# Kernel tuning notes

Measured on AMD Instinct MI355X. Metric: run time of the kernel, lower is better.

The kernel has to match this reference:

```python
import jax, jax.numpy as jnp
import numpy as np

EMBED_DIM = 1024
NUM_HEADS = 16
HEAD_DIM = EMBED_DIM // NUM_HEADS
BATCH = 2
SEQ = 2048


def setup_inputs() -> dict:
    key = jax.random.key(0)
    ks = jax.random.split(key, 10)
    s = 1.0 / np.sqrt(EMBED_DIM)
    inp = {
        "query": jax.random.normal(ks[0], (BATCH, SEQ, EMBED_DIM), jnp.float32),
        # Linear weights stored as [in, out] (y = x @ W + b)
        "wq": jax.random.normal(ks[1], (EMBED_DIM, EMBED_DIM), jnp.float32) * s,
        "bq": jnp.zeros((EMBED_DIM,), jnp.float32),
        "wk": jax.random.normal(ks[2], (EMBED_DIM, EMBED_DIM), jnp.float32) * s,
        "bk": jnp.zeros((EMBED_DIM,), jnp.float32),
        "wv": jax.random.normal(ks[3], (EMBED_DIM, EMBED_DIM), jnp.float32) * s,
        "bv": jnp.zeros((EMBED_DIM,), jnp.float32),
        "wo": jax.random.normal(ks[4], (EMBED_DIM, EMBED_DIM), jnp.float32) * s,
        "bo": jnp.zeros((EMBED_DIM,), jnp.float32),
        "temperature": jnp.float32(HEAD_DIM),  # learnable temperature, init = head_dim
    }
    return inp


def reference(query, wq, bq, wk, bk, wv, bv, wo, bo, temperature):
    B, S, E = query.shape
    # self-attention: key = value = query
    Q = (query @ wq + bq).reshape(B, S, NUM_HEADS, HEAD_DIM).transpose(0, 2, 1, 3)
    K = (query @ wk + bk).reshape(B, S, NUM_HEADS, HEAD_DIM).transpose(0, 2, 1, 3)
    V = (query @ wv + bv).reshape(B, S, NUM_HEADS, HEAD_DIM).transpose(0, 2, 1, 3)
    # squared Euclidean distances: ||q||^2 + ||k||^2 - 2<q,k>
    q_sq = jnp.sum(Q * Q, axis=-1, keepdims=True)          # (B,H,Sq,1)
    k_sq = jnp.sum(K * K, axis=-1, keepdims=True)          # (B,H,Sk,1)
    qk = jnp.einsum("bhqd,bhkd->bhqk", Q, K)
    d_sq = jnp.maximum(q_sq + jnp.swapaxes(k_sq, -2, -1) - 2.0 * qk, 0.0)
    attn = jax.nn.softmax(-d_sq / temperature, axis=-1)    # (B,H,Sq,Sk)
    out = jnp.einsum("bhqk,bhkd->bhqd", attn, V)
    out = out.transpose(0, 2, 1, 3).reshape(B, S, E)
    return out @ wo + bo
```

## Files before the change

### kernel.cpp

```cpp
#include <hip/hip_runtime.h>
#include <stdint.h>
#include <stddef.h>


#define LOG2E 1.44269504088896f

typedef __attribute__((ext_vector_type(8))) short bf16x8;
typedef __attribute__((ext_vector_type(4))) float f32x4;
typedef __attribute__((ext_vector_type(4))) unsigned short u16x4;

__device__ __forceinline__ unsigned short f2b(float f) {
  union { float f; unsigned int u; } x; x.f = f;
  unsigned int u = x.u;
  u += 0x7fffu + ((u >> 16) & 1u);
  return (unsigned short)(u >> 16);
}
__device__ __forceinline__ float b2f(unsigned short s) {
  union { unsigned int u; float f; } x; x.u = ((unsigned int)s) << 16;
  return x.f;
}
__device__ __forceinline__ unsigned int fbits(float f) {
  union { float f; unsigned int u; } x; x.f = f; return x.u;
}

#define GLD_LDS(g, l) __builtin_amdgcn_global_load_lds( \
    (const __attribute__((address_space(1))) void*)(g), \
    (__attribute__((address_space(3))) void*)(l), 16, 0, 0)

__global__ void prep_kernel(const float* __restrict__ X,
                            const float* __restrict__ wq, const float* __restrict__ wk,
                            const float* __restrict__ wv, const float* __restrict__ wo,
                            unsigned short* __restrict__ Xb,
                            unsigned short* __restrict__ WTqkv, unsigned short* __restrict__ WTo) {
  int z = blockIdx.z;
  if (z == 4) {
    size_t base = ((size_t)(blockIdx.y * 16 + blockIdx.x)) * 16384;
    #pragma unroll
    for (int j = 0; j < 16; ++j) {
      size_t i = base + (size_t)(j * 256 + threadIdx.x) * 4;
      f32x4 v = *(const f32x4*)&X[i];
      u16x4 o;
      #pragma unroll
      for (int k = 0; k < 4; ++k) o[k] = f2b(v[k]);
      *(u16x4*)&Xb[i] = o;
    }
    return;
  }
  __shared__ float tile[64][65];
  const float* src = (z == 0) ? wq : (z == 1) ? wk : (z == 2) ? wv : wo;
  unsigned short* dst = (z < 3) ? (WTqkv + (size_t)z * 1024 * 1024) : WTo;
  int k0 = blockIdx.y * 64, n0 = blockIdx.x * 64;
  int rr = threadIdx.x >> 6, cc = threadIdx.x & 63;
  #pragma unroll
  for (int p = 0; p < 16; ++p) {
    int row = p * 4 + rr;
    tile[row][cc] = src[(size_t)(k0 + row) * 1024 + n0 + cc];
  }
  __syncthreads();
  #pragma unroll
  for (int p = 0; p < 16; ++p) {
    int row = p * 4 + rr;
    dst[(size_t)(n0 + row) * 1024 + k0 + cc] = f2b(tile[cc][row]);
  }
}

__global__ __launch_bounds__(256, 3) void gemm_qkv_kernel(
    const unsigned short* __restrict__ X, const unsigned short* __restrict__ WT,
    const float* __restrict__ bq, const float* __restrict__ bk, const float* __restrict__ bv,
    const float* __restrict__ temp,
    unsigned short* __restrict__ Qb, unsigned short* __restrict__ Kb,
    unsigned short* __restrict__ VTo, float* __restrict__ ks2) {
  __shared__ __align__(16) unsigned short smem[16896];
  unsigned short* As = smem;
  unsigned short* Bs = smem + 8192;
  const int t = threadIdx.x, w = t >> 6, lane = t & 63;
  const int r = lane & 15, q4 = lane >> 4;
  const int m0 = blockIdx.y * 128, n0 = blockIdx.x * 128;
  const int wr = (w >> 1) * 64, wc = (w & 1) * 64;
  const unsigned short* Xg = X + (size_t)m0 * 1024;
  const unsigned short* Wg = WT + (size_t)n0 * 1024;
  f32x4 acc[4][4] = {};
  for (int k0 = 0; k0 < 1024; k0 += 64) {
    #pragma unroll
    for (int g = 0; g < 4; ++g) {
      int slot = g * 256 + t;
      int kh = slot >> 9, row = (slot >> 2) & 127, ko = (slot & 3) * 8;
      GLD_LDS(Xg + (size_t)row * 1024 + k0 + kh * 32 + ko, &As[(g * 256 + w * 64) * 8]);
      GLD_LDS(Wg + (size_t)row * 1024 + k0 + kh * 32 + ko, &Bs[(g * 256 + w * 64) * 8]);
    }
    __syncthreads();
    #pragma unroll
    for (int kh = 0; kh < 2; ++kh) {
      bf16x8 af[4], bfr[4];
      #pragma unroll
      for (int mf = 0; mf < 4; ++mf)
        af[mf] = *(const bf16x8*)&As[kh * 4096 + (wr + mf * 16 + r) * 32 + q4 * 8];
      #pragma unroll
      for (int nf = 0; nf < 4; ++nf)
        bfr[nf] = *(const bf16x8*)&Bs[kh * 4096 + (wc + nf * 16 + r) * 32 + q4 * 8];
      #pragma unroll
      for (int mf = 0; mf < 4; ++mf)
        #pragma unroll
        for (int nf = 0; nf < 4; ++nf)
          acc[mf][nf] = __builtin_amdgcn_mfma_f32_16x16x32_bf16(af[mf], bfr[nf], acc[mf][nf], 0, 0, 0);
    }
    __syncthreads();
  }
  const int nblk = n0 >> 10;
  if (nblk == 0) {
    const int nc0 = n0 & 1023;
    #pragma unroll
    for (int nf = 0; nf < 4; ++nf) {
      int n = nc0 + wc + nf * 16 + r;
      float bb = bq[n];
      #pragma unroll
      for (int mf = 0; mf < 4; ++mf) {
        int m = m0 + wr + mf * 16 + q4 * 4;
        f32x4 v = acc[mf][nf];
        #pragma unroll
        for (int i = 0; i < 4; ++i)
          Qb[(size_t)(m + i) * 1024 + n] = f2b(v[i] + bb);
      }
    }
  } else if (nblk == 1) {
    const float sc = LOG2E / temp[0];
    const int nc0 = n0 & 1023;
    float s2a[4][4] = {};
    #pragma unroll
    for (int nf = 0; nf < 4; ++nf) {
      int n = nc0 + wc + nf * 16 + r;
      float bb = bk[n];
      #pragma unroll
      for (int mf = 0; mf < 4; ++mf) {
        int m = m0 + wr + mf * 16 + q4 * 4;
        f32x4 v = acc[mf][nf];
        #pragma unroll
        for (int i = 0; i < 4; ++i) {
          unsigned short os = f2b(v[i] + bb);
          Kb[(size_t)(m + i) * 1024 + n] = os;
          float xb = b2f(os);
          s2a[mf][i] += xb * xb;
        }
      }
    }
    #pragma unroll
    for (int mf = 0; mf < 4; ++mf)
      #pragma unroll
      for (int i = 0; i < 4; ++i) {
        float v = s2a[mf][i];
        v += __shfl_xor(v, 1, 64);
        v += __shfl_xor(v, 2, 64);
        v += __shfl_xor(v, 4, 64);
        v += __shfl_xor(v, 8, 64);
        s2a[mf][i] = v * sc;
      }
    if (r == 0) {
      int hh = (nc0 + wc) >> 6;
      #pragma unroll
      for (int mf = 0; mf < 4; ++mf) {
        int m = m0 + wr + mf * 16 + q4 * 4;
        int bb2 = m >> 11, ss = m & 2047;
        #pragma unroll
        for (int i = 0; i < 4; ++i)
          ks2[(size_t)(bb2 * 16 + hh) * 2048 + ss + i] = s2a[mf][i];
      }
    }
  } else {
    unsigned short* Vt = smem;
    const int c0 = n0 - 2048;
    const int head = w & 1;
    #pragma unroll
    for (int nf = 0; nf < 4; ++nf) {
      int c = c0 + wc + nf * 16 + r;
      float bb = bv[c];
      int d = c & 63;
      #pragma unroll
      for (int mf = 0; mf < 4; ++mf) {
        int mloc = wr + mf * 16 + q4 * 4;
        int G = mloc >> 6;
        int k6 = mloc & 63;
        int pos = (k6 >> 5) * 32 + ((k6 & 15) >> 2) * 8 + ((k6 >> 4) & 1) * 4;
        f32x4 v = acc[mf][nf];
        u16x4 pk;
        #pragma unroll
        for (int i = 0; i < 4; ++i) pk[i] = f2b(v[i] + bb);
        *(u16x4*)&Vt[(head * 64 + d) * 132 + G * 64 + pos] = pk;
      }
    }
    __syncthreads();
    int row = t >> 1, ch = t & 1;
    int hd = row >> 6, dd = row & 63;
    int hglob = (c0 >> 6) + hd;
    int bb2 = m0 >> 11, s0 = m0 & 2047;
    unsigned short* dst = &VTo[((size_t)((bb2 * 16 + hglob) * 64 + dd)) * 2048 + s0 + ch * 64];
    const unsigned short* srcL = &Vt[(hd * 64 + dd) * 132 + ch * 64];
    #pragma unroll
    for (int k2 = 0; k2 < 16; ++k2)
      *(u16x4*)&dst[k2 * 4] = *(const u16x4*)&srcL[k2 * 4];
  }
}

__global__ __launch_bounds__(256, 2) void flash_kernel(
    const unsigned short* __restrict__ Qb, const unsigned short* __restrict__ Kb,
    const unsigned short* __restrict__ VT, const float* __restrict__ ks2,
    const float* __restrict__ temp, unsigned short* __restrict__ AO) {
  __shared__ __align__(16) unsigned short Ks[2][64 * 64];
  __shared__ __align__(16) unsigned short Vs[3][64 * 64];
  __shared__ __align__(16) float KQs[2048];
  const int t = threadIdx.x, w = t >> 6, lane = t & 63;
  const int r = lane & 15, q4 = lane >> 4;
  const int wgid = blockIdx.x + 16 * blockIdx.y;
  const int xcd = wgid & 7, s = wgid >> 3;
  const int bh = xcd + 8 * (s & 3);
  const int b = bh >> 4, h = bh & 15;
  const int q0 = (s >> 2) * 128;
  const float cc = 2.0f * LOG2E / temp[0];

  bf16x8 qf[2][2];
  #pragma unroll
  for (int qg = 0; qg < 2; ++qg) {
    int sq = q0 + w * 32 + qg * 16 + r;
    const unsigned short* qp = Qb + (size_t)(b * 2048 + sq) * 1024 + h * 64;
    #pragma unroll
    for (int ks = 0; ks < 2; ++ks) qf[qg][ks] = *(const bf16x8*)(qp + ks * 32 + q4 * 8);
  }

  f32x4 accO[2][4] = {};
  f32x4 lsum[2] = {};
  bf16x8 ones;
  #pragma unroll
  for (int j = 0; j < 8; ++j) ones[j] = (short)0x3F80;

  const unsigned short* Kg = Kb + ((size_t)b * 2048) * 1024 + h * 64;
  const unsigned short* Vg = VT + ((size_t)bh * 64) * 2048;
  const float* kqb = ks2 + bh * 2048;

  const unsigned short* kp0 = Kg + (size_t)(t >> 2) * 1024 + (t & 3) * 8;
  const unsigned short* kp1 = kp0 + 32;
  int dd0 = t >> 3;
  const unsigned short* vp0 = Vg + (size_t)dd0 * 2048 + ((t & 7) ^ (dd0 & 7)) * 8;
  const unsigned short* vp1 = vp0 + (size_t)32 * 2048;

  GLD_LDS(kqb + t * 4, &KQs[t * 4]);
  GLD_LDS(kqb + 1024 + t * 4, &KQs[1024 + t * 4]);
  GLD_LDS(kp0, &Ks[0][t * 8]);
  GLD_LDS(kp1, &Ks[0][(256 + t) * 8]);
  GLD_LDS(vp0, &Vs[0][t * 8]);
  GLD_LDS(vp1, &Vs[0][(256 + t) * 8]);
  kp0 += 65536; kp1 += 65536; vp0 += 64; vp1 += 64;
  GLD_LDS(kp0, &Ks[1][t * 8]);
  GLD_LDS(kp1, &Ks[1][(256 + t) * 8]);
  GLD_LDS(vp0, &Vs[1][t * 8]);
  GLD_LDS(vp1, &Vs[1][(256 + t) * 8]);
  kp0 += 65536; kp1 += 65536; vp0 += 64; vp1 += 64;

  const unsigned short* v_cur = &Vs[0][0];
  const unsigned short* v_nxt = &Vs[1][0];
  const unsigned short* v_fre = &Vs[2][0];

  asm volatile("s_waitcnt vmcnt(4)" ::: "memory");
  __builtin_amdgcn_s_barrier();
  __builtin_amdgcn_sched_barrier(0);

  f32x4 stA[2][4], stB[2][4];
  {
    const f32x4 zz = {};
    __builtin_amdgcn_s_setprio(1);
    #pragma unroll
    for (int ks = 0; ks < 2; ++ks) {
      #pragma unroll
      for (int kfm = 0; kfm < 4; ++kfm) {
        bf16x8 ka = *(const bf16x8*)&Ks[0][(ks * 64 + kfm * 16 + r) * 32 + q4 * 8];
        stA[0][kfm] = __builtin_amdgcn_mfma_f32_16x16x32_bf16(ka, qf[0][ks], ks ? stA[0][kfm] : zz, 0, 0, 0);
        stA[1][kfm] = __builtin_amdgcn_mfma_f32_16x16x32_bf16(ka, qf[1][ks], ks ? stA[1][kfm] : zz, 0, 0, 0);
      }
    }
    __builtin_amdgcn_s_setprio(0);
  }

#define CHUNK_BODY(C, STC, STN)                                               \
  {                                                                           \
    const int c_ = (C);                                                       \
    __builtin_amdgcn_s_barrier();                                             \
    if (c_ < 30) {                                                            \
      unsigned short* kdst = &Ks[(C) & 1][0];                                 \
      GLD_LDS(kp0, kdst + t * 8);                                             \
      GLD_LDS(kp1, kdst + (256 + t) * 8);                                     \
      GLD_LDS(vp0, (unsigned short*)v_fre + t * 8);                           \
      GLD_LDS(vp1, (unsigned short*)v_fre + (256 + t) * 8);                   \
      kp0 += 65536; kp1 += 65536; vp0 += 64; vp1 += 64;                       \
      asm volatile("s_waitcnt vmcnt(4)" ::: "memory");                        \
    } else {                                                                  \
      asm volatile("s_waitcnt vmcnt(0)" ::: "memory");                        \
    }                                                                         \
    __builtin_amdgcn_s_barrier();                                             \
    __builtin_amdgcn_sched_barrier(0);                                        \
                 \
    if (c_ < 31) {                                                            \
      const unsigned short* krd = &Ks[((C) + 1) & 1][0];                      \
      const f32x4 zz = {};                                                    \
      __builtin_amdgcn_s_setprio(1);                                          \
      _Pragma("unroll")                                                       \
      for (int ks = 0; ks < 2; ++ks) {                                        \
        _Pragma("unroll")                                                     \
        for (int kfm = 0; kfm < 4; ++kfm) {                                   \
          bf16x8 ka = *(const bf16x8*)&krd[(ks * 64 + kfm * 16 + r) * 32 + q4 * 8]; \
          STN[0][kfm] = __builtin_amdgcn_mfma_f32_16x16x32_bf16(ka, qf[0][ks], ks ? STN[0][kfm] : zz, 0, 0, 0); \
          STN[1][kfm] = __builtin_amdgcn_mfma_f32_16x16x32_bf16(ka, qf[1][ks], ks ? STN[1][kfm] : zz, 0, 0, 0); \
        }                                                                     \
      }                                                                       \
      __builtin_amdgcn_s_setprio(0);                                          \
    }                                                                         \
                                \
    f32x4 kq[4];                                                              \
    _Pragma("unroll")                                                         \
    for (int kfm = 0; kfm < 4; ++kfm)                                         \
      kq[kfm] = *(const f32x4*)&KQs[c_ * 64 + kfm * 16 + q4 * 4];             \
    bf16x8 pf[2][2];                                                          \
    _Pragma("unroll")                                                         \
    for (int qg = 0; qg < 2; ++qg) {                                          \
      _Pragma("unroll")                                                       \
      for (int cb = 0; cb < 2; ++cb) {                                        \
        unsigned int dw[4];                                                   \
        _Pragma("unroll")                                                     \
        for (int half = 0; half < 2; ++half) {                                \
          int kfm = cb * 2 + half;                                            \
          float pp[4];                                                        \
          _Pragma("unroll")                                                   \
          for (int i = 0; i < 4; ++i) {                                       \
            float u = __builtin_fmaf(cc, STC[qg][kfm][i], -kq[kfm][i]);       \
            pp[i] = __builtin_amdgcn_exp2f(u);                                \
          }                                                                   \
          dw[half * 2 + 0] = (fbits(pp[0]) >> 16) | (fbits(pp[1]) & 0xFFFF0000u); \
          dw[half * 2 + 1] = (fbits(pp[2]) >> 16) | (fbits(pp[3]) & 0xFFFF0000u); \
        }                                                                     \
        union { unsigned int d[4]; bf16x8 v; } cv;                            \
        cv.d[0] = dw[0]; cv.d[1] = dw[1]; cv.d[2] = dw[2]; cv.d[3] = dw[3];   \
        pf[qg][cb] = cv.v;                                                    \
      }                                                                       \
    }                                                                         \
        \
    __builtin_amdgcn_s_setprio(1);                                            \
    _Pragma("unroll")                                                         \
    for (int cb = 0; cb < 2; ++cb) {                                          \
      lsum[0] = __builtin_amdgcn_mfma_f32_16x16x32_bf16(pf[0][cb], ones, lsum[0], 0, 0, 0); \
      lsum[1] = __builtin_amdgcn_mfma_f32_16x16x32_bf16(pf[1][cb], ones, lsum[1], 0, 0, 0); \
      _Pragma("unroll")                                                       \
      for (int df = 0; df < 4; ++df) {                                        \
        int dloc = df * 16 + r;                                               \
        int un = dloc * 8 + ((cb * 4 + q4) ^ (dloc & 7));                     \
        bf16x8 vb = *(const bf16x8*)&v_cur[un * 8];                           \
        accO[0][df] = __builtin_amdgcn_mfma_f32_16x16x32_bf16(pf[0][cb], vb, accO[0][df], 0, 0, 0); \
        accO[1][df] = __builtin_amdgcn_mfma_f32_16x16x32_bf16(pf[1][cb], vb, accO[1][df], 0, 0, 0); \
      }                                                                       \
    }                                                                         \
    __builtin_amdgcn_s_setprio(0);                                            \
                                                        \
    const unsigned short* tv = v_cur; v_cur = v_nxt; v_nxt = v_fre; v_fre = tv; \
  }

  for (int c2 = 0; c2 < 16; ++c2) {
    CHUNK_BODY(2 * c2, stA, stB)
    CHUNK_BODY(2 * c2 + 1, stB, stA)
  }
#undef CHUNK_BODY

  {
    #pragma unroll
    for (int qg = 0; qg < 2; ++qg) {
      float inv[4];
      #pragma unroll
      for (int i = 0; i < 4; ++i) inv[i] = 1.0f / lsum[qg][i];
      #pragma unroll
      for (int df = 0; df < 4; ++df) {
        int d = df * 16 + r;
        #pragma unroll
        for (int i = 0; i < 4; ++i) {
          int sq = q0 + w * 32 + qg * 16 + q4 * 4 + i;
          AO[(size_t)(b * 2048 + sq) * 1024 + h * 64 + d] = f2b(accO[qg][df][i] * inv[i]);
        }
      }
    }
  }
}

__global__ __launch_bounds__(256, 2) void gemm_out_kernel(
    const unsigned short* __restrict__ A, const unsigned short* __restrict__ WT,
    const float* __restrict__ bo, float* __restrict__ Out) {
  __shared__ __align__(16) unsigned short As[2 * 128 * 32];
  __shared__ __align__(16) unsigned short Bs[2 * 64 * 32];
  const int t = threadIdx.x, w = t >> 6, lane = t & 63;
  const int r = lane & 15, q4 = lane >> 4;
  const int m0 = blockIdx.y * 128, n0 = blockIdx.x * 64;
  const int wr = (w >> 1) * 64, wc = (w & 1) * 32;
  const unsigned short* Ag = A + (size_t)m0 * 1024;
  const unsigned short* Wg = WT + (size_t)n0 * 1024;
  f32x4 acc[4][2] = {};
  for (int k0 = 0; k0 < 1024; k0 += 64) {
    #pragma unroll
    for (int g = 0; g < 4; ++g) {
      int slot = g * 256 + t;
      int kh = slot >> 9, row = (slot >> 2) & 127, ko = (slot & 3) * 8;
      GLD_LDS(Ag + (size_t)row * 1024 + k0 + kh * 32 + ko, &As[(g * 256 + w * 64) * 8]);
    }
    #pragma unroll
    for (int g = 0; g < 2; ++g) {
      int slot = g * 256 + t;
      int kh = slot >> 8, row = (slot >> 2) & 63, ko = (slot & 3) * 8;
      GLD_LDS(Wg + (size_t)row * 1024 + k0 + kh * 32 + ko, &Bs[(g * 256 + w * 64) * 8]);
    }
    __syncthreads();
    #pragma unroll
    for (int kh = 0; kh < 2; ++kh) {
      bf16x8 af[4], bfr[2];
      #pragma unroll
      for (int mf = 0; mf < 4; ++mf)
        af[mf] = *(const bf16x8*)&As[kh * 4096 + (wr + mf * 16 + r) * 32 + q4 * 8];
      #pragma unroll
      for (int nf = 0; nf < 2; ++nf)
        bfr[nf] = *(const bf16x8*)&Bs[kh * 2048 + (wc + nf * 16 + r) * 32 + q4 * 8];
      #pragma unroll
      for (int mf = 0; mf < 4; ++mf)
        #pragma unroll
        for (int nf = 0; nf < 2; ++nf)
          acc[mf][nf] = __builtin_amdgcn_mfma_f32_16x16x32_bf16(af[mf], bfr[nf], acc[mf][nf], 0, 0, 0);
    }
    __syncthreads();
  }
  #pragma unroll
  for (int nf = 0; nf < 2; ++nf) {
    int n = n0 + wc + nf * 16 + r;
    float bb = bo[n];
    #pragma unroll
    for (int mf = 0; mf < 4; ++mf) {
      int m = m0 + wr + mf * 16 + q4 * 4;
      f32x4 v = acc[mf][nf];
      #pragma unroll
      for (int i = 0; i < 4; ++i)
        Out[(size_t)(m + i) * 1024 + n] = v[i] + bb;
    }
  }
}

extern "C" void kernel_launch(void* const* d_in, const int* in_sizes, int n_in,
                              void* d_out, int out_size, void* d_ws, size_t ws_size,
                              hipStream_t stream) {
  const float* X    = (const float*)d_in[0];
  const float* wq   = (const float*)d_in[1];
  const float* bq   = (const float*)d_in[2];
  const float* wk   = (const float*)d_in[3];
  const float* bk   = (const float*)d_in[4];
  const float* wv   = (const float*)d_in[5];
  const float* bv   = (const float*)d_in[6];
  const float* wo   = (const float*)d_in[7];
  const float* bo   = (const float*)d_in[8];
  const float* temp = (const float*)d_in[9];
  float* Out = (float*)d_out;

  char* ws = (char*)d_ws;
  unsigned short* Xb    = (unsigned short*)ws; ws += (size_t)4096 * 1024 * 2;
  unsigned short* WTqkv = (unsigned short*)ws; ws += (size_t)3072 * 1024 * 2;
  unsigned short* WTo   = (unsigned short*)ws; ws += (size_t)1024 * 1024 * 2;
  unsigned short* Qb    = (unsigned short*)ws; ws += (size_t)4096 * 1024 * 2;
  unsigned short* Kb    = (unsigned short*)ws; ws += (size_t)4096 * 1024 * 2;
  unsigned short* VT    = (unsigned short*)ws; ws += (size_t)4096 * 1024 * 2;
  float* ks2 = (float*)ws; ws += (size_t)65536 * 4;
  unsigned short* AO = Xb;

  prep_kernel<<<dim3(16, 16, 5), 256, 0, stream>>>(X, wq, wk, wv, wo, Xb, WTqkv, WTo);
  gemm_qkv_kernel<<<dim3(24, 32), 256, 0, stream>>>(Xb, WTqkv, bq, bk, bv, temp, Qb, Kb, VT, ks2);
  flash_kernel<<<dim3(16, 32), 256, 0, stream>>>(Qb, Kb, VT, ks2, temp, AO);
  gemm_out_kernel<<<dim3(16, 32), 256, 0, stream>>>(AO, WTo, bo, Out);
}
```

Before: 189.1 us.

## Double flash query tile to 256 rows with 4-stage K/V pipeline

The flash kernel now gives each block 256 query rows (64 per wave) instead of 128, which halves the grid and halves how often K/V tiles are reloaded per query. K and V staging moves to a 4-deep ring buffer with 3 chunks prefetched, and the software-pipelined QK^T (computing the next chunk's scores early) is dropped in favour of computing scores within the same chunk. Launch bounds drop to one block per SIMD set, so register pressure and occupancy change. The grid shrinks to 256 blocks, which may underfill the GPU's compute units.

```diff
diff --git a/kernel.cpp b/kernel.cpp
--- a/kernel.cpp
+++ b/kernel.cpp
@@ -200,33 +200,33 @@
   }
 }
 
-__global__ __launch_bounds__(256, 2) void flash_kernel(
+__global__ __launch_bounds__(256, 1) void flash_kernel(
     const unsigned short* __restrict__ Qb, const unsigned short* __restrict__ Kb,
     const unsigned short* __restrict__ VT, const float* __restrict__ ks2,
     const float* __restrict__ temp, unsigned short* __restrict__ AO) {
-  __shared__ __align__(16) unsigned short Ks[2][64 * 64];
-  __shared__ __align__(16) unsigned short Vs[3][64 * 64];
+  __shared__ __align__(16) unsigned short Ks[4][64 * 64];
+  __shared__ __align__(16) unsigned short Vs[4][64 * 64];
   __shared__ __align__(16) float KQs[2048];
   const int t = threadIdx.x, w = t >> 6, lane = t & 63;
   const int r = lane & 15, q4 = lane >> 4;
-  const int wgid = blockIdx.x + 16 * blockIdx.y;
+  const int wgid = blockIdx.x + 8 * blockIdx.y;
   const int xcd = wgid & 7, s = wgid >> 3;
   const int bh = xcd + 8 * (s & 3);
   const int b = bh >> 4, h = bh & 15;
-  const int q0 = (s >> 2) * 128;
+  const int q0 = (s >> 2) * 256;
   const float cc = 2.0f * LOG2E / temp[0];
 
-  bf16x8 qf[2][2];
-  #pragma unroll
-  for (int qg = 0; qg < 2; ++qg) {
-    int sq = q0 + w * 32 + qg * 16 + r;
+  bf16x8 qf[4][2];
+  #pragma unroll
+  for (int qg = 0; qg < 4; ++qg) {
+    int sq = q0 + w * 64 + qg * 16 + r;
     const unsigned short* qp = Qb + (size_t)(b * 2048 + sq) * 1024 + h * 64;
     #pragma unroll
     for (int ks = 0; ks < 2; ++ks) qf[qg][ks] = *(const bf16x8*)(qp + ks * 32 + q4 * 8);
   }
 
-  f32x4 accO[2][4] = {};
-  f32x4 lsum[2] = {};
+  f32x4 accO[4][4] = {};
+  f32x4 lsum[4] = {};
   bf16x8 ones;
   #pragma unroll
   for (int j = 0; j < 8; ++j) ones[j] = (short)0x3F80;
@@ -243,82 +243,51 @@
 
   GLD_LDS(kqb + t * 4, &KQs[t * 4]);
   GLD_LDS(kqb + 1024 + t * 4, &KQs[1024 + t * 4]);
-  GLD_LDS(kp0, &Ks[0][t * 8]);
-  GLD_LDS(kp1, &Ks[0][(256 + t) * 8]);
-  GLD_LDS(vp0, &Vs[0][t * 8]);
-  GLD_LDS(vp1, &Vs[0][(256 + t) * 8]);
-  kp0 += 65536; kp1 += 65536; vp0 += 64; vp1 += 64;
-  GLD_LDS(kp0, &Ks[1][t * 8]);
-  GLD_LDS(kp1, &Ks[1][(256 + t) * 8]);
-  GLD_LDS(vp0, &Vs[1][t * 8]);
-  GLD_LDS(vp1, &Vs[1][(256 + t) * 8]);
-  kp0 += 65536; kp1 += 65536; vp0 += 64; vp1 += 64;
-
-  const unsigned short* v_cur = &Vs[0][0];
-  const unsigned short* v_nxt = &Vs[1][0];
-  const unsigned short* v_fre = &Vs[2][0];
-
-  asm volatile("s_waitcnt vmcnt(4)" ::: "memory");
+  #pragma unroll
+  for (int pc = 0; pc < 3; ++pc) {
+    GLD_LDS(kp0, &Ks[pc][t * 8]);
+    GLD_LDS(kp1, &Ks[pc][(256 + t) * 8]);
+    GLD_LDS(vp0, &Vs[pc][t * 8]);
+    GLD_LDS(vp1, &Vs[pc][(256 + t) * 8]);
+    kp0 += 65536; kp1 += 65536; vp0 += 64; vp1 += 64;
+  }
+  asm volatile("s_waitcnt vmcnt(8)" ::: "memory");
   __builtin_amdgcn_s_barrier();
   __builtin_amdgcn_sched_barrier(0);
 
-  f32x4 stA[2][4], stB[2][4];
-  {
-    const f32x4 zz = {};
-    __builtin_amdgcn_s_setprio(1);
-    #pragma unroll
-    for (int ks = 0; ks < 2; ++ks) {
-      #pragma unroll
-      for (int kfm = 0; kfm < 4; ++kfm) {
-        bf16x8 ka = *(const bf16x8*)&Ks[0][(ks * 64 + kfm * 16 + r) * 32 + q4 * 8];
-        stA[0][kfm] = __builtin_amdgcn_mfma_f32_16x16x32_bf16(ka, qf[0][ks], ks ? stA[0][kfm] : zz, 0, 0, 0);
-        stA[1][kfm] = __builtin_amdgcn_mfma_f32_16x16x32_bf16(ka, qf[1][ks], ks ? stA[1][kfm] : zz, 0, 0, 0);
-      }
-    }
-    __builtin_amdgcn_s_setprio(0);
-  }
-
-#define CHUNK_BODY(C, STC, STN)                                               \
+#define CHUNK_BODY(C, J)                                                      \
   {                                                                           \
     const int c_ = (C);                                                       \
-    __builtin_amdgcn_s_barrier();                                             \
-    if (c_ < 30) {                                                            \
-      unsigned short* kdst = &Ks[(C) & 1][0];                                 \
-      GLD_LDS(kp0, kdst + t * 8);                                             \
-      GLD_LDS(kp1, kdst + (256 + t) * 8);                                     \
-      GLD_LDS(vp0, (unsigned short*)v_fre + t * 8);                           \
-      GLD_LDS(vp1, (unsigned short*)v_fre + (256 + t) * 8);                   \
+    if (c_ < 29) {                                                            \
+      GLD_LDS(kp0, &Ks[((J) + 3) & 3][t * 8]);                                \
+      GLD_LDS(kp1, &Ks[((J) + 3) & 3][(256 + t) * 8]);                        \
+      GLD_LDS(vp0, &Vs[((J) + 3) & 3][t * 8]);                                \
+      GLD_LDS(vp1, &Vs[((J) + 3) & 3][(256 + t) * 8]);                        \
       kp0 += 65536; kp1 += 65536; vp0 += 64; vp1 += 64;                       \
-      asm volatile("s_waitcnt vmcnt(4)" ::: "memory");                        \
-    } else {                                                                  \
-      asm volatile("s_waitcnt vmcnt(0)" ::: "memory");                        \
     }                                                                         \
-    __builtin_amdgcn_s_barrier();                                             \
-    __builtin_amdgcn_sched_barrier(0);                                        \
-                 \
-    if (c_ < 31) {                                                            \
-      const unsigned short* krd = &Ks[((C) + 1) & 1][0];                      \
+         \
+    f32x4 st[4][4];                                                           \
+    {                                                                         \
       const f32x4 zz = {};                                                    \
-      __builtin_amdgcn_s_setprio(1);                                          \
       _Pragma("unroll")                                                       \
       for (int ks = 0; ks < 2; ++ks) {                                        \
         _Pragma("unroll")                                                     \
         for (int kfm = 0; kfm < 4; ++kfm) {                                   \
-          bf16x8 ka = *(const bf16x8*)&krd[(ks * 64 + kfm * 16 + r) * 32 + q4 * 8]; \
-          STN[0][kfm] = __builtin_amdgcn_mfma_f32_16x16x32_bf16(ka, qf[0][ks], ks ? STN[0][kfm] : zz, 0, 0, 0); \
-          STN[1][kfm] = __builtin_amdgcn_mfma_f32_16x16x32_bf16(ka, qf[1][ks], ks ? STN[1][kfm] : zz, 0, 0, 0); \
+          bf16x8 ka = *(const bf16x8*)&Ks[(J)][(ks * 64 + kfm * 16 + r) * 32 + q4 * 8]; \
+          _Pragma("unroll")                                                   \
+          for (int qg = 0; qg < 4; ++qg)                                      \
+            st[qg][kfm] = __builtin_amdgcn_mfma_f32_16x16x32_bf16(ka, qf[qg][ks], ks ? st[qg][kfm] : zz, 0, 0, 0); \
         }                                                                     \
       }                                                                       \
-      __builtin_amdgcn_s_setprio(0);                                          \
     }                                                                         \
-                                \
+                 \
     f32x4 kq[4];                                                              \
     _Pragma("unroll")                                                         \
     for (int kfm = 0; kfm < 4; ++kfm)                                         \
       kq[kfm] = *(const f32x4*)&KQs[c_ * 64 + kfm * 16 + q4 * 4];             \
-    bf16x8 pf[2][2];                                                          \
+    bf16x8 pf[4][2];                                                          \
     _Pragma("unroll")                                                         \
-    for (int qg = 0; qg < 2; ++qg) {                                          \
+    for (int qg = 0; qg < 4; ++qg) {                                          \
       _Pragma("unroll")                                                       \
       for (int cb = 0; cb < 2; ++cb) {                                        \
         unsigned int dw[4];                                                   \
@@ -328,7 +297,7 @@
           float pp[4];                                                        \
           _Pragma("unroll")                                                   \
           for (int i = 0; i < 4; ++i) {                                       \
-            float u = __builtin_fmaf(cc, STC[qg][kfm][i], -kq[kfm][i]);       \
+            float u = __builtin_fmaf(cc, st[qg][kfm][i], -kq[kfm][i]);        \
             pp[i] = __builtin_amdgcn_exp2f(u);                                \
           }                                                                   \
           dw[half * 2 + 0] = (fbits(pp[0]) >> 16) | (fbits(pp[1]) & 0xFFFF0000u); \
@@ -339,35 +308,41 @@
         pf[qg][cb] = cv.v;                                                    \
       }                                                                       \
     }                                                                         \
-        \
-    __builtin_amdgcn_s_setprio(1);                                            \
+         \
     _Pragma("unroll")                                                         \
     for (int cb = 0; cb < 2; ++cb) {                                          \
-      lsum[0] = __builtin_amdgcn_mfma_f32_16x16x32_bf16(pf[0][cb], ones, lsum[0], 0, 0, 0); \
-      lsum[1] = __builtin_amdgcn_mfma_f32_16x16x32_bf16(pf[1][cb], ones, lsum[1], 0, 0, 0); \
+      _Pragma("unroll")                                                       \
+      for (int qg = 0; qg < 4; ++qg)                                          \
+        lsum[qg] = __builtin_amdgcn_mfma_f32_16x16x32_bf16(pf[qg][cb], ones, lsum[qg], 0, 0, 0); \
       _Pragma("unroll")                                                       \
       for (int df = 0; df < 4; ++df) {                                        \
         int dloc = df * 16 + r;                                               \
         int un = dloc * 8 + ((cb * 4 + q4) ^ (dloc & 7));                     \
-        bf16x8 vb = *(const bf16x8*)&v_cur[un * 8];                           \
-        accO[0][df] = __builtin_amdgcn_mfma_f32_16x16x32_bf16(pf[0][cb], vb, accO[0][df], 0, 0, 0); \
-        accO[1][df] = __builtin_amdgcn_mfma_f32_16x16x32_bf16(pf[1][cb], vb, accO[1][df], 0, 0, 0); \
+        bf16x8 vb = *(const bf16x8*)&Vs[(J)][un * 8];                         \
+        _Pragma("unroll")                                                     \
+        for (int qg = 0; qg < 4; ++qg)                                        \
+          accO[qg][df] = __builtin_amdgcn_mfma_f32_16x16x32_bf16(pf[qg][cb], vb, accO[qg][df], 0, 0, 0); \
       }                                                                       \
     }                                                                         \
-    __builtin_amdgcn_s_setprio(0);                                            \
-                                                        \
-    const unsigned short* tv = v_cur; v_cur = v_nxt; v_nxt = v_fre; v_fre = tv; \
-  }
-
-  for (int c2 = 0; c2 < 16; ++c2) {
-    CHUNK_BODY(2 * c2, stA, stB)
-    CHUNK_BODY(2 * c2 + 1, stB, stA)
+                \
+    if (c_ < 29)      { asm volatile("s_waitcnt vmcnt(8)" ::: "memory"); }    \
+    else if (c_ == 29){ asm volatile("s_waitcnt vmcnt(4)" ::: "memory"); }    \
+    else              { asm volatile("s_waitcnt vmcnt(0)" ::: "memory"); }    \
+    __builtin_amdgcn_s_barrier();                                             \
+    __builtin_amdgcn_sched_barrier(0);                                        \
+  }
+
+  for (int c4 = 0; c4 < 8; ++c4) {
+    CHUNK_BODY(4 * c4 + 0, 0)
+    CHUNK_BODY(4 * c4 + 1, 1)
+    CHUNK_BODY(4 * c4 + 2, 2)
+    CHUNK_BODY(4 * c4 + 3, 3)
   }
 #undef CHUNK_BODY
 
   {
     #pragma unroll
-    for (int qg = 0; qg < 2; ++qg) {
+    for (int qg = 0; qg < 4; ++qg) {
       float inv[4];
       #pragma unroll
       for (int i = 0; i < 4; ++i) inv[i] = 1.0f / lsum[qg][i];
@@ -376,7 +351,7 @@
         int d = df * 16 + r;
         #pragma unroll
         for (int i = 0; i < 4; ++i) {
-          int sq = q0 + w * 32 + qg * 16 + q4 * 4 + i;
+          int sq = q0 + w * 64 + qg * 16 + q4 * 4 + i;
           AO[(size_t)(b * 2048 + sq) * 1024 + h * 64 + d] = f2b(accO[qg][df][i] * inv[i]);
         }
       }
@@ -469,6 +444,6 @@
 
   prep_kernel<<<dim3(16, 16, 5), 256, 0, stream>>>(X, wq, wk, wv, wo, Xb, WTqkv, WTo);
   gemm_qkv_kernel<<<dim3(24, 32), 256, 0, stream>>>(Xb, WTqkv, bq, bk, bv, temp, Qb, Kb, VT, ks2);
-  flash_kernel<<<dim3(16, 32), 256, 0, stream>>>(Qb, Kb, VT, ks2, temp, AO);
+  flash_kernel<<<dim3(8, 32), 256, 0, stream>>>(Qb, Kb, VT, ks2, temp, AO);
   gemm_out_kernel<<<dim3(16, 32), 256, 0, stream>>>(AO, WTo, bo, Out);
 }
```

Result: no change. 192.6 us (+1.9%).

## Triple-buffer QKV and output GEMM K-loops with async global-to-LDS prefetch

Applied to the files above, without the earlier changes.

Both projection GEMMs now use a three-stage LDS ring over 32-wide K slices. Loads for slice k+2 are issued before computing slice k, and each step waits with a partial vmcnt and a single barrier. This hides global load latency behind MFMA work and replaces two syncthreads per K step with one. The cost is more LDS per block (48KB vs 33KB for QKV), which may reduce occupancy, plus fragile hand-written waitcnt bookkeeping.

```diff
diff --git a/kernel.cpp b/kernel.cpp
--- a/kernel.cpp
+++ b/kernel.cpp
@@ -70,42 +70,69 @@
     const float* __restrict__ temp,
     unsigned short* __restrict__ Qb, unsigned short* __restrict__ Kb,
     unsigned short* __restrict__ VTo, float* __restrict__ ks2) {
-  __shared__ __align__(16) unsigned short smem[16896];
-  unsigned short* As = smem;
-  unsigned short* Bs = smem + 8192;
+  __shared__ __align__(16) unsigned short smem3[24576];
+#define AS3(j) (smem3 + (j) * 4096)
+#define BS3(j) (smem3 + 12288 + (j) * 4096)
   const int t = threadIdx.x, w = t >> 6, lane = t & 63;
   const int r = lane & 15, q4 = lane >> 4;
   const int m0 = blockIdx.y * 128, n0 = blockIdx.x * 128;
   const int wr = (w >> 1) * 64, wc = (w & 1) * 64;
   const unsigned short* Xg = X + (size_t)m0 * 1024;
   const unsigned short* Wg = WT + (size_t)n0 * 1024;
+  const unsigned short* xs0 = Xg + (size_t)(t >> 2) * 1024 + (t & 3) * 8;
+  const unsigned short* xs1 = xs0 + (size_t)64 * 1024;
+  const unsigned short* ws0 = Wg + (size_t)(t >> 2) * 1024 + (t & 3) * 8;
+  const unsigned short* ws1 = ws0 + (size_t)64 * 1024;
   f32x4 acc[4][4] = {};
-  for (int k0 = 0; k0 < 1024; k0 += 64) {
-    #pragma unroll
-    for (int g = 0; g < 4; ++g) {
-      int slot = g * 256 + t;
-      int kh = slot >> 9, row = (slot >> 2) & 127, ko = (slot & 3) * 8;
-      GLD_LDS(Xg + (size_t)row * 1024 + k0 + kh * 32 + ko, &As[(g * 256 + w * 64) * 8]);
-      GLD_LDS(Wg + (size_t)row * 1024 + k0 + kh * 32 + ko, &Bs[(g * 256 + w * 64) * 8]);
-    }
-    __syncthreads();
-    #pragma unroll
-    for (int kh = 0; kh < 2; ++kh) {
-      bf16x8 af[4], bfr[4];
-      #pragma unroll
-      for (int mf = 0; mf < 4; ++mf)
-        af[mf] = *(const bf16x8*)&As[kh * 4096 + (wr + mf * 16 + r) * 32 + q4 * 8];
-      #pragma unroll
-      for (int nf = 0; nf < 4; ++nf)
-        bfr[nf] = *(const bf16x8*)&Bs[kh * 4096 + (wc + nf * 16 + r) * 32 + q4 * 8];
-      #pragma unroll
-      for (int mf = 0; mf < 4; ++mf)
-        #pragma unroll
-        for (int nf = 0; nf < 4; ++nf)
-          acc[mf][nf] = __builtin_amdgcn_mfma_f32_16x16x32_bf16(af[mf], bfr[nf], acc[mf][nf], 0, 0, 0);
-    }
-    __syncthreads();
-  }
+
+#define QKV_STAGE(J2)                                     \
+  {                                                       \
+    GLD_LDS(xs0, &AS3(J2)[(w * 64) * 8]);                 \
+    GLD_LDS(xs1, &AS3(J2)[(256 + w * 64) * 8]);           \
+    GLD_LDS(ws0, &BS3(J2)[(w * 64) * 8]);                 \
+    GLD_LDS(ws1, &BS3(J2)[(256 + w * 64) * 8]);           \
+    xs0 += 32; xs1 += 32; ws0 += 32; ws1 += 32;           \
+  }
+
+  QKV_STAGE(0)
+  QKV_STAGE(1)
+  asm volatile("s_waitcnt vmcnt(4)" ::: "memory");
+  __builtin_amdgcn_s_barrier();
+  __builtin_amdgcn_sched_barrier(0);
+
+#define QKV_BODY(J, STG, LAST)                                                \
+  {                                                                           \
+    if (STG) QKV_STAGE(((J) + 2) % 3)                                         \
+    bf16x8 af[4], bfr[4];                                                     \
+    _Pragma("unroll")                                                         \
+    for (int mf = 0; mf < 4; ++mf)                                            \
+      af[mf] = *(const bf16x8*)&AS3(J)[(wr + mf * 16 + r) * 32 + q4 * 8];     \
+    _Pragma("unroll")                                                         \
+    for (int nf = 0; nf < 4; ++nf)                                            \
+      bfr[nf] = *(const bf16x8*)&BS3(J)[(wc + nf * 16 + r) * 32 + q4 * 8];    \
+    _Pragma("unroll")                                                         \
+    for (int mf = 0; mf < 4; ++mf)                                            \
+      _Pragma("unroll")                                                       \
+      for (int nf = 0; nf < 4; ++nf)                                          \
+        acc[mf][nf] = __builtin_amdgcn_mfma_f32_16x16x32_bf16(af[mf], bfr[nf], acc[mf][nf], 0, 0, 0); \
+    if (STG)       { asm volatile("s_waitcnt vmcnt(4)" ::: "memory"); }       \
+    else if (!(LAST)) { asm volatile("s_waitcnt vmcnt(0)" ::: "memory"); }    \
+    if (!(LAST)) {                                                            \
+      __builtin_amdgcn_s_barrier();                                           \
+      __builtin_amdgcn_sched_barrier(0);                                      \
+    }                                                                         \
+  }
+
+  for (int hh = 0; hh < 5; ++hh) {
+    QKV_BODY(0, 1, 0) QKV_BODY(1, 1, 0) QKV_BODY(2, 1, 0)
+    QKV_BODY(0, 1, 0) QKV_BODY(1, 1, 0) QKV_BODY(2, 1, 0)
+  }
+  QKV_BODY(0, 0, 0)
+  QKV_BODY(1, 0, 1)
+  __syncthreads();
+#undef QKV_BODY
+#undef QKV_STAGE
+
   const int nblk = n0 >> 10;
   if (nblk == 0) {
     const int nc0 = n0 & 1023;
@@ -155,18 +182,18 @@
         s2a[mf][i] = v * sc;
       }
     if (r == 0) {
-      int hh = (nc0 + wc) >> 6;
+      int hh2 = (nc0 + wc) >> 6;
       #pragma unroll
       for (int mf = 0; mf < 4; ++mf) {
         int m = m0 + wr + mf * 16 + q4 * 4;
         int bb2 = m >> 11, ss = m & 2047;
         #pragma unroll
         for (int i = 0; i < 4; ++i)
-          ks2[(size_t)(bb2 * 16 + hh) * 2048 + ss + i] = s2a[mf][i];
+          ks2[(size_t)(bb2 * 16 + hh2) * 2048 + ss + i] = s2a[mf][i];
       }
     }
   } else {
-    unsigned short* Vt = smem;
+    unsigned short* Vt = smem3;
     const int c0 = n0 - 2048;
     const int head = w & 1;
     #pragma unroll
@@ -198,6 +225,8 @@
     for (int k2 = 0; k2 < 16; ++k2)
       *(u16x4*)&dst[k2 * 4] = *(const u16x4*)&srcL[k2 * 4];
   }
+#undef AS3
+#undef BS3
 }
 
 __global__ __launch_bounds__(256, 2) void flash_kernel(
@@ -355,7 +384,6 @@
       }                                                                       \
     }                                                                         \
     __builtin_amdgcn_s_setprio(0);                                            \
-                                                        \
     const unsigned short* tv = v_cur; v_cur = v_nxt; v_nxt = v_fre; v_fre = tv; \
   }
 
@@ -387,46 +415,68 @@
 __global__ __launch_bounds__(256, 2) void gemm_out_kernel(
     const unsigned short* __restrict__ A, const unsigned short* __restrict__ WT,
     const float* __restrict__ bo, float* __restrict__ Out) {
-  __shared__ __align__(16) unsigned short As[2 * 128 * 32];
-  __shared__ __align__(16) unsigned short Bs[2 * 64 * 32];
+  __shared__ __align__(16) unsigned short osmem[18432];
+#define AS3o(j) (osmem + (j) * 4096)
+#define BS3o(j) (osmem + 12288 + (j) * 2048)
   const int t = threadIdx.x, w = t >> 6, lane = t & 63;
   const int r = lane & 15, q4 = lane >> 4;
   const int m0 = blockIdx.y * 128, n0 = blockIdx.x * 64;
   const int wr = (w >> 1) * 64, wc = (w & 1) * 32;
   const unsigned short* Ag = A + (size_t)m0 * 1024;
   const unsigned short* Wg = WT + (size_t)n0 * 1024;
+  const unsigned short* as0 = Ag + (size_t)(t >> 2) * 1024 + (t & 3) * 8;
+  const unsigned short* as1 = as0 + (size_t)64 * 1024;
+  const unsigned short* bs0 = Wg + (size_t)(t >> 2) * 1024 + (t & 3) * 8;
   f32x4 acc[4][2] = {};
-  for (int k0 = 0; k0 < 1024; k0 += 64) {
-    #pragma unroll
-    for (int g = 0; g < 4; ++g) {
-      int slot = g * 256 + t;
-      int kh = slot >> 9, row = (slot >> 2) & 127, ko = (slot & 3) * 8;
-      GLD_LDS(Ag + (size_t)row * 1024 + k0 + kh * 32 + ko, &As[(g * 256 + w * 64) * 8]);
-    }
-    #pragma unroll
-    for (int g = 0; g < 2; ++g) {
-      int slot = g * 256 + t;
-      int kh = slot >> 8, row = (slot >> 2) & 63, ko = (slot & 3) * 8;
-      GLD_LDS(Wg + (size_t)row * 1024 + k0 + kh * 32 + ko, &Bs[(g * 256 + w * 64) * 8]);
-    }
-    __syncthreads();
-    #pragma unroll
-    for (int kh = 0; kh < 2; ++kh) {
-      bf16x8 af[4], bfr[2];
-      #pragma unroll
-      for (int mf = 0; mf < 4; ++mf)
-        af[mf] = *(const bf16x8*)&As[kh * 4096 + (wr + mf * 16 + r) * 32 + q4 * 8];
-      #pragma unroll
-      for (int nf = 0; nf < 2; ++nf)
-        bfr[nf] = *(const bf16x8*)&Bs[kh * 2048 + (wc + nf * 16 + r) * 32 + q4 * 8];
-      #pragma unroll
-      for (int mf = 0; mf < 4; ++mf)
-        #pragma unroll
-        for (int nf = 0; nf < 2; ++nf)
-          acc[mf][nf] = __builtin_amdgcn_mfma_f32_16x16x32_bf16(af[mf], bfr[nf], acc[mf][nf], 0, 0, 0);
-    }
-    __syncthreads();
-  }
+
+#define OUT_STAGE(J2)                                     \
+  {                                                       \
+    GLD_LDS(as0, &AS3o(J2)[(w * 64) * 8]);                \
+    GLD_LDS(as1, &AS3o(J2)[(256 + w * 64) * 8]);          \
+    GLD_LDS(bs0, &BS3o(J2)[(w * 64) * 8]);                \
+    as0 += 32; as1 += 32; bs0 += 32;                      \
+  }
+
+  OUT_STAGE(0)
+  OUT_STAGE(1)
+  asm volatile("s_waitcnt vmcnt(3)" ::: "memory");
+  __builtin_amdgcn_s_barrier();
+  __builtin_amdgcn_sched_barrier(0);
+
+#define OUT_BODY(J, STG, LAST)                                                \
+  {                                                                           \
+    if (STG) OUT_STAGE(((J) + 2) % 3)                                         \
+    bf16x8 af[4], bfr[2];                                                     \
+    _Pragma("unroll")                                                         \
+    for (int mf = 0; mf < 4; ++mf)                                            \
+      af[mf] = *(const bf16x8*)&AS3o(J)[(wr + mf * 16 + r) * 32 + q4 * 8];    \
+    _Pragma("unroll")                                                         \
+    for (int nf = 0; nf < 2; ++nf)                                            \
+      bfr[nf] = *(const bf16x8*)&BS3o(J)[(wc + nf * 16 + r) * 32 + q4 * 8];   \
+    _Pragma("unroll")                                                         \
+    for (int mf = 0; mf < 4; ++mf)                                            \
+      _Pragma("unroll")                                                       \
+      for (int nf = 0; nf < 2; ++nf)                                          \
+        acc[mf][nf] = __builtin_amdgcn_mfma_f32_16x16x32_bf16(af[mf], bfr[nf], acc[mf][nf], 0, 0, 0); \
+    if (STG)       { asm volatile("s_waitcnt vmcnt(3)" ::: "memory"); }       \
+    else if (!(LAST)) { asm volatile("s_waitcnt vmcnt(0)" ::: "memory"); }    \
+    if (!(LAST)) {                                                            \
+      __builtin_amdgcn_s_barrier();                                           \
+      __builtin_amdgcn_sched_barrier(0);                                      \
+    }                                                                         \
+  }
+
+  for (int hh = 0; hh < 5; ++hh) {
+    OUT_BODY(0, 1, 0) OUT_BODY(1, 1, 0) OUT_BODY(2, 1, 0)
+    OUT_BODY(0, 1, 0) OUT_BODY(1, 1, 0) OUT_BODY(2, 1, 0)
+  }
+  OUT_BODY(0, 0, 0)
+  OUT_BODY(1, 0, 1)
+#undef OUT_BODY
+#undef OUT_STAGE
+#undef AS3o
+#undef BS3o
+
   #pragma unroll
   for (int nf = 0; nf < 2; ++nf) {
     int n = n0 + wc + nf * 16 + r;
```

After: 184.9 us. 2.2% less time.
